# Optimization experiments

Hardware: AMD Instinct MI355X
Metric: run time of the kernel (lower is better)

Reference implementation:

```python
import jax, jax.numpy as jnp
import numpy as np

N_NODES = 50000
EPS = 1e-5


def gcn_conv(x, edge_index, edge_weight, W, b, n):
    # PyG GCNConv: h = x @ W; out[dst] += norm * h[src]; out += b
    # with self-loops (weight 1) and symmetric normalization D^-1/2 A D^-1/2.
    src, dst = edge_index[0], edge_index[1]
    loop = jnp.arange(n)
    src_all = jnp.concatenate([src, loop])            # [E+N]
    dst_all = jnp.concatenate([dst, loop])
    w_all = jnp.concatenate([edge_weight, jnp.ones((n,), x.dtype)])
    deg = jax.ops.segment_sum(w_all, dst_all, num_segments=n)
    dinv = jnp.where(deg > 0, jax.lax.rsqrt(jnp.maximum(deg, 1e-30)), 0.0)
    norm = dinv[src_all] * w_all * dinv[dst_all]      # [E+N]
    h = x @ W                                         # [N, out]
    msg = h[src_all] * norm[:, None]                  # [E+N, out]
    return jax.ops.segment_sum(msg, dst_all, num_segments=n) + b


def setup_inputs() -> dict:
    key = jax.random.key(0)
    ks = jax.random.split(key, 8)
    nfeat, nhid, nout = 1024, 256, 256
    E = 800000
    x = jax.random.normal(ks[0], (N_NODES, nfeat), dtype=jnp.float32)
    edge_index = jax.random.randint(ks[1], (2, E), 0, N_NODES, dtype=jnp.int64)
    edge_weight = jax.random.uniform(ks[2], (E,), dtype=jnp.float32)
    W1 = jax.random.normal(ks[3], (nfeat, nhid), dtype=jnp.float32) / np.sqrt(nfeat)
    b1 = jnp.zeros((nhid,), jnp.float32)
    W2 = jax.random.normal(ks[4], (nhid, nout), dtype=jnp.float32) / np.sqrt(nhid)
    b2 = jnp.zeros((nout,), jnp.float32)
    bn_gamma = jnp.ones((nout,), jnp.float32)
    bn_beta = jnp.zeros((nout,), jnp.float32)
    ln_gamma = jnp.ones((nout,), jnp.float32)
    ln_beta = jnp.zeros((nout,), jnp.float32)
    return {"x": x, "edge_index": edge_index, "edge_weight": edge_weight,
            "W1": W1, "b1": b1, "W2": W2, "b2": b2,
            "bn_gamma": bn_gamma, "bn_beta": bn_beta,
            "ln_gamma": ln_gamma, "ln_beta": ln_beta}


def reference(x, edge_index, edge_weight, W1, b1, W2, b2,
              bn_gamma, bn_beta, ln_gamma, ln_beta):
    n = x.shape[0]
    # dropout is identity in eval mode
    h = jax.nn.relu(gcn_conv(x, edge_index, edge_weight, W1, b1, n))
    h = jax.nn.relu(gcn_conv(h, edge_index, edge_weight, W2, b2, n))
    # BatchNorm1d (training-mode batch statistics, biased variance)
    mu = jnp.mean(h, axis=0)
    var = jnp.mean((h - mu) ** 2, axis=0)
    h = (h - mu) * jax.lax.rsqrt(var + EPS) * bn_gamma + bn_beta
    # LayerNorm over feature dim
    lmu = jnp.mean(h, axis=-1, keepdims=True)
    lvar = jnp.mean((h - lmu) ** 2, axis=-1, keepdims=True)
    return (h - lmu) * jax.lax.rsqrt(lvar + EPS) * ln_gamma + ln_beta
```

## Files before the change

kernel.cpp:

```cpp
#include <hip/hip_runtime.h>


typedef __attribute__((ext_vector_type(4))) float f32x4;
typedef __attribute__((ext_vector_type(8))) _Float16 f16x8;
typedef __attribute__((ext_vector_type(4))) _Float16 f16x4;

#define NN 50000
#define NF 1024
#define NH 256

__global__ __launch_bounds__(256) void deg_count(const int* __restrict__ ei,
    const float* __restrict__ ew, unsigned long long* __restrict__ dc, int E)
{
    int e = blockIdx.x * 256 + threadIdx.x;
    if (e >= E) return;
    int d = ei[E + e];
    unsigned long long pack = (1ull << 40) |
        (unsigned long long)(unsigned int)(ew[e] * 16777216.0f + 0.5f);
    atomicAdd(&dc[d], pack);
}

__global__ __launch_bounds__(256) void dinv_k(const unsigned long long* __restrict__ dc,
    float* __restrict__ dinv, int n)
{
    int i = blockIdx.x * 256 + threadIdx.x;
    if (i < n) {
        float deg = (float)(dc[i] & 0xFFFFFFFFFFull) * (1.0f / 16777216.0f);
        dinv[i] = rsqrtf(deg + 1.0f);
    }
}

__global__ __launch_bounds__(512) void scan_a(const unsigned long long* __restrict__ dc,
    int* __restrict__ excl, int* __restrict__ bsum, int n)
{
    __shared__ int sm[512];
    int t = threadIdx.x, g = blockIdx.x * 512 + t;
    int v = (g < n) ? (int)(dc[g] >> 40) : 0;
    sm[t] = v;
    __syncthreads();
    for (int d = 1; d < 512; d <<= 1) {
        int x = (t >= d) ? sm[t - d] : 0;
        __syncthreads();
        sm[t] += x;
        __syncthreads();
    }
    if (g < n) excl[g] = sm[t] - v;
    if (t == 511) bsum[blockIdx.x] = sm[511];
}

__global__ __launch_bounds__(128) void scan_b(int* __restrict__ bsum, int nb)
{
    __shared__ int sm[128];
    int t = threadIdx.x;
    int v = (t < nb) ? bsum[t] : 0;
    sm[t] = v;
    __syncthreads();
    for (int d = 1; d < 128; d <<= 1) {
        int x = (t >= d) ? sm[t - d] : 0;
        __syncthreads();
        sm[t] += x;
        __syncthreads();
    }
    if (t < nb) bsum[t] = sm[t] - v;
}

__global__ __launch_bounds__(256) void scan_c(const int* __restrict__ excl,
    const int* __restrict__ bsum, int* __restrict__ offs, int n, int E)
{
    int g = blockIdx.x * 256 + threadIdx.x;
    if (g < n) offs[g] = excl[g] + bsum[g >> 9];
    else if (g == n) offs[n] = E;
}

__global__ __launch_bounds__(256) void scatter_k(const int* __restrict__ ei,
    const float* __restrict__ ew, const int* __restrict__ offs,
    int* __restrict__ cursor, const float* __restrict__ dinv,
    int* __restrict__ csrc, float* __restrict__ cwv, int E)
{
    int e = blockIdx.x * 256 + threadIdx.x;
    if (e >= E) return;
    int s = ei[e], d = ei[E + e];
    int pos = offs[d] + atomicAdd(&cursor[d], 1);
    csrc[pos] = s;
    cwv[pos] = ew[e] * dinv[s] * dinv[d];
}

__global__ __launch_bounds__(256) void cvt_w(const float* __restrict__ W,
    unsigned short* __restrict__ WT, int K, int total)
{
    int idx = blockIdx.x * 256 + threadIdx.x;
    if (idx >= total) return;
    int k = idx >> 8, n = idx & 255;
    ((_Float16*)WT)[(size_t)n * K + k] = (_Float16)W[idx];
}

template<bool AF32>
__global__ __launch_bounds__(256, 2) void gemm_pipe(
    const void* __restrict__ Av, const unsigned short* __restrict__ BT,
    _Float16* __restrict__ C, int M, int K)
{
    constexpr int LS = 40;
    __shared__ _Float16 As[2][128 * LS];
    __shared__ _Float16 Bs[2][128 * LS];
    const int t = threadIdx.x;
    const int lane = t & 63, wid = t >> 6;
    const int r = lane & 15, q = lane >> 4;
    const int n0 = blockIdx.x * 128;
    const int m0 = blockIdx.y * 128;
    const int wm = (wid >> 1) * 64, wn = (wid & 1) * 64;
    const float* Af = (const float*)Av;
    const _Float16* Ah = (const _Float16*)Av;

    int rowA32[4], rowA16[2];
#pragma unroll
    for (int it = 0; it < 4; ++it) {
        int m = it * 32 + (t >> 3);
        int gm = m0 + m; if (gm >= M) gm = M - 1;
        rowA32[it] = gm;
    }
#pragma unroll
    for (int it = 0; it < 2; ++it) {
        int m = it * 64 + (t >> 2);
        int gm = m0 + m; if (gm >= M) gm = M - 1;
        rowA16[it] = gm;
    }
    const int kcA32 = (t & 7) << 2;
    const int kcA16 = (t & 3) << 3;
    const int nB = (t >> 2) & 63;
    const int kcB = (t & 3) << 3;

    f32x4 acc[4][4];
#pragma unroll
    for (int i = 0; i < 4; ++i)
#pragma unroll
        for (int j = 0; j < 4; ++j) acc[i][j] = (f32x4){0.f, 0.f, 0.f, 0.f};

    f32x4 apre[2][4][2];
    f16x8 aph[2][2];
    f16x8 bpre[2][2];

    const int T = K >> 5;

#define G_ISSUE_A(kt, p)                                                        \
    {                                                                           \
        if constexpr (AF32) {                                                   \
            _Pragma("unroll")                                                   \
            for (int it = 0; it < 4; ++it) {                                    \
                const float* g = Af + (size_t)rowA32[it] * K + ((kt) << 5) + kcA32; \
                apre[p][it][0] = *(const f32x4*)g;                              \
            }                                                                   \
        } else {                                                                \
            _Pragma("unroll")                                                   \
            for (int it = 0; it < 2; ++it)                                      \
                aph[p][it] = *(const f16x8*)(Ah + (size_t)rowA16[it] * K + ((kt) << 5) + kcA16); \
        }                                                                       \
    }

#define G_ISSUE_B(kt, p)                                                        \
    {                                                                           \
        _Pragma("unroll")                                                       \
        for (int rd = 0; rd < 2; ++rd)                                          \
            bpre[p][rd] = *(const f16x8*)((const _Float16*)BT +                 \
                (size_t)(n0 + rd * 64 + nB) * K + ((kt) << 5) + kcB);           \
    }

#define G_STAGE(p)                                                              \
    {                                                                           \
        if constexpr (AF32) {                                                   \
            _Pragma("unroll")                                                   \
            for (int it = 0; it < 4; ++it) {                                    \
                int m = it * 32 + (t >> 3);                                     \
                f16x4 hv;                                                       \
                hv.x = (_Float16)apre[p][it][0].x;                              \
                hv.y = (_Float16)apre[p][it][0].y;                              \
                hv.z = (_Float16)apre[p][it][0].z;                              \
                hv.w = (_Float16)apre[p][it][0].w;                              \
                *(f16x4*)(&As[p][0] + m * LS + kcA32) = hv;                     \
            }                                                                   \
        } else {                                                                \
            _Pragma("unroll")                                                   \
            for (int it = 0; it < 2; ++it) {                                    \
                int m = it * 64 + (t >> 2);                                     \
                *(f16x8*)(&As[p][0] + m * LS + kcA16) = aph[p][it];             \
            }                                                                   \
        }                                                                       \
        _Pragma("unroll")                                                       \
        for (int rd = 0; rd < 2; ++rd) {                                        \
            int n = rd * 64 + (t >> 2);                                         \
            *(f16x8*)(&Bs[p][0] + n * LS + kcB) = bpre[p][rd];                  \
        }                                                                       \
    }


#define G_BODY(kk, p)                                                           \
    {                                                                           \
        G_STAGE(p);                                                             \
        asm volatile("s_waitcnt lgkmcnt(0)" ::: "memory");                      \
        __builtin_amdgcn_s_barrier();                                           \
        __builtin_amdgcn_sched_barrier(0);                                      \
        if ((kk) + 2 < T) { G_ISSUE_A((kk) + 2, p); G_ISSUE_B((kk) + 2, p); }   \
        __builtin_amdgcn_sched_barrier(0);                                      \
        f16x8 af[4], bf[4];                                                     \
        _Pragma("unroll")                                                       \
        for (int i = 0; i < 4; ++i)                                             \
            af[i] = *(const f16x8*)(&As[p][0] + (wm + i * 16 + r) * LS + q * 8); \
        _Pragma("unroll")                                                       \
        for (int j = 0; j < 4; ++j)                                             \
            bf[j] = *(const f16x8*)(&Bs[p][0] + (wn + j * 16 + r) * LS + q * 8); \
        _Pragma("unroll")                                                       \
        for (int i = 0; i < 4; ++i)                                             \
            _Pragma("unroll")                                                   \
            for (int j = 0; j < 4; ++j)                                         \
                acc[i][j] = __builtin_amdgcn_mfma_f32_16x16x32_f16(af[i], bf[j], acc[i][j], 0, 0, 0); \
        __builtin_amdgcn_sched_barrier(0);                                      \
    }

    G_ISSUE_A(0, 0); G_ISSUE_B(0, 0);
    G_ISSUE_A(1, 1); G_ISSUE_B(1, 1);

    for (int k = 0; k < T; k += 2) {
        G_BODY(k, 0);
        G_BODY(k + 1, 1);
    }

#pragma unroll
    for (int i = 0; i < 4; ++i) {
#pragma unroll
        for (int reg = 0; reg < 4; ++reg) {
            int m = m0 + wm + i * 16 + q * 4 + reg;
            if (m < M) {
                _Float16* cp = C + (size_t)m * 256 + (n0 + wn + r);
#pragma unroll
                for (int j = 0; j < 4; ++j) cp[j * 16] = (_Float16)acc[i][j][reg];
            }
        }
    }
#undef G_ISSUE_A
#undef G_ISSUE_B
#undef G_STAGE
#undef G_BODY
}

__global__ __launch_bounds__(256) void agg_relu(
    const _Float16* __restrict__ h, const int* __restrict__ roff,
    const int* __restrict__ csrc, const float* __restrict__ cwv,
    const float* __restrict__ dinv, const float* __restrict__ bias,
    _Float16* __restrict__ out, int n)
{
    const int lane = threadIdx.x & 63, wid = threadIdx.x >> 6;
    const int i = blockIdx.x * 4 + wid;
    if (i >= n) return;
    const int c = lane << 2;
    const float di = dinv[i];
    const float sw = di * di;
    const f16x4 hv = *(const f16x4*)(h + (size_t)i * 256 + c);
    float a0 = sw * (float)hv.x, a1 = sw * (float)hv.y;
    float a2 = sw * (float)hv.z, a3 = sw * (float)hv.w;
    float b0 = 0.f, b1 = 0.f, b2 = 0.f, b3 = 0.f;
    float c0 = 0.f, c1 = 0.f, c2 = 0.f, c3 = 0.f;
    float d0 = 0.f, d1 = 0.f, d2 = 0.f, d3 = 0.f;
    const int p0 = roff[i], pe = roff[i + 1];
    for (int base = p0; base < pe; base += 64) {
        int lim = pe - base; if (lim > 64) lim = 64;
        int sv = 0; float wv = 0.f;
        if (lane < lim) { sv = csrc[base + lane]; wv = cwv[base + lane]; }
        int j = 0;
        for (; j + 3 < lim; j += 4) {
            int s0 = __shfl(sv, j),     s1 = __shfl(sv, j + 1);
            int s2 = __shfl(sv, j + 2), s3 = __shfl(sv, j + 3);
            float w0 = __shfl(wv, j),     w1 = __shfl(wv, j + 1);
            float w2 = __shfl(wv, j + 2), w3 = __shfl(wv, j + 3);
            f16x4 v0 = *(const f16x4*)(h + (size_t)s0 * 256 + c);
            f16x4 v1 = *(const f16x4*)(h + (size_t)s1 * 256 + c);
            f16x4 v2 = *(const f16x4*)(h + (size_t)s2 * 256 + c);
            f16x4 v3 = *(const f16x4*)(h + (size_t)s3 * 256 + c);
            a0 += w0 * (float)v0.x; a1 += w0 * (float)v0.y;
            a2 += w0 * (float)v0.z; a3 += w0 * (float)v0.w;
            b0 += w1 * (float)v1.x; b1 += w1 * (float)v1.y;
            b2 += w1 * (float)v1.z; b3 += w1 * (float)v1.w;
            c0 += w2 * (float)v2.x; c1 += w2 * (float)v2.y;
            c2 += w2 * (float)v2.z; c3 += w2 * (float)v2.w;
            d0 += w3 * (float)v3.x; d1 += w3 * (float)v3.y;
            d2 += w3 * (float)v3.z; d3 += w3 * (float)v3.w;
        }
        for (; j < lim; ++j) {
            int s0 = __shfl(sv, j);
            float w0 = __shfl(wv, j);
            f16x4 v0 = *(const f16x4*)(h + (size_t)s0 * 256 + c);
            a0 += w0 * (float)v0.x; a1 += w0 * (float)v0.y;
            a2 += w0 * (float)v0.z; a3 += w0 * (float)v0.w;
        }
    }
    const float4 bb = *(const float4*)(bias + c);
    f16x4 o;
    o.x = (_Float16)fmaxf(a0 + b0 + c0 + d0 + bb.x, 0.f);
    o.y = (_Float16)fmaxf(a1 + b1 + c1 + d1 + bb.y, 0.f);
    o.z = (_Float16)fmaxf(a2 + b2 + c2 + d2 + bb.z, 0.f);
    o.w = (_Float16)fmaxf(a3 + b3 + c3 + d3 + bb.w, 0.f);
    *(f16x4*)(out + (size_t)i * 256 + c) = o;
}

__global__ __launch_bounds__(256) void bn_stats(const _Float16* __restrict__ h,
    float* __restrict__ bnsum, float* __restrict__ bnsq, int n)
{
    const int t = threadIdx.x;
    float s = 0.f, s2 = 0.f;
    for (int r = blockIdx.x; r < n; r += gridDim.x) {
        float v = (float)h[(size_t)r * 256 + t];
        s += v; s2 += v * v;
    }
    atomicAdd(&bnsum[t], s);
    atomicAdd(&bnsq[t], s2);
}

__global__ __launch_bounds__(256) void bn_params(const float* __restrict__ bnsum,
    const float* __restrict__ bnsq, const float* __restrict__ gamma,
    const float* __restrict__ beta, float* __restrict__ scale,
    float* __restrict__ shift, int n)
{
    int t = threadIdx.x;
    float mu = bnsum[t] / (float)n;
    float var = bnsq[t] / (float)n - mu * mu;
    float sc = gamma[t] * rsqrtf(var + 1e-5f);
    scale[t] = sc;
    shift[t] = beta[t] - mu * sc;
}

__global__ __launch_bounds__(256) void bn_ln(const _Float16* __restrict__ h,
    const float* __restrict__ scale, const float* __restrict__ shift,
    const float* __restrict__ lng, const float* __restrict__ lnb,
    float* __restrict__ out, int n)
{
    const int lane = threadIdx.x & 63, wid = threadIdx.x >> 6;
    const int i = blockIdx.x * 4 + wid;
    if (i >= n) return;
    const int c = lane << 2;
    const f16x4 v = *(const f16x4*)(h + (size_t)i * 256 + c);
    const float4 sc = *(const float4*)(scale + c);
    const float4 sh = *(const float4*)(shift + c);
    float y0 = (float)v.x * sc.x + sh.x;
    float y1 = (float)v.y * sc.y + sh.y;
    float y2 = (float)v.z * sc.z + sh.z;
    float y3 = (float)v.w * sc.w + sh.w;
    float ps = y0 + y1 + y2 + y3;
    float ps2 = y0 * y0 + y1 * y1 + y2 * y2 + y3 * y3;
#pragma unroll
    for (int off = 32; off > 0; off >>= 1) {
        ps += __shfl_down(ps, off);
        ps2 += __shfl_down(ps2, off);
    }
    ps = __shfl(ps, 0);
    ps2 = __shfl(ps2, 0);
    const float mu = ps * (1.f / 256.f);
    const float var = ps2 * (1.f / 256.f) - mu * mu;
    const float rs = rsqrtf(var + 1e-5f);
    const float4 g = *(const float4*)(lng + c);
    const float4 bb = *(const float4*)(lnb + c);
    float4 o;
    o.x = (y0 - mu) * rs * g.x + bb.x;
    o.y = (y1 - mu) * rs * g.y + bb.y;
    o.z = (y2 - mu) * rs * g.z + bb.z;
    o.w = (y3 - mu) * rs * g.w + bb.w;
    *(float4*)(out + (size_t)i * 256 + c) = o;
}

extern "C" void kernel_launch(void* const* d_in, const int* in_sizes, int n_in,
                              void* d_out, int out_size, void* d_ws, size_t ws_size,
                              hipStream_t stream)
{
    const float* x   = (const float*)d_in[0];
    const int*   ei  = (const int*)d_in[1];
    const float* ew  = (const float*)d_in[2];
    const float* W1  = (const float*)d_in[3];
    const float* b1  = (const float*)d_in[4];
    const float* W2  = (const float*)d_in[5];
    const float* b2  = (const float*)d_in[6];
    const float* bng = (const float*)d_in[7];
    const float* bnb = (const float*)d_in[8];
    const float* lng = (const float*)d_in[9];
    const float* lnb = (const float*)d_in[10];
    float* out = (float*)d_out;

    const int N = NN;
    const int E = in_sizes[2];

    char* ws = (char*)d_ws;
    size_t o = 0;
    auto alloc = [&](size_t b) -> char* {
        char* p = ws + o;
        o = (o + b + 255) & ~(size_t)255;
        return p;
    };
    _Float16* h1  = (_Float16*)alloc((size_t)N * NH * 2);
    _Float16* h1a = (_Float16*)alloc((size_t)N * NH * 2);
    _Float16* h2a = (_Float16*)alloc((size_t)N * NH * 2);
    unsigned short* W1T = (unsigned short*)alloc((size_t)NH * NF * 2);
    unsigned short* W2T = (unsigned short*)alloc((size_t)NH * NH * 2);
    int*   csrc = (int*)alloc((size_t)E * 4);
    float* cwv  = (float*)alloc((size_t)E * 4);
    int*   offs = (int*)alloc((size_t)(N + 1) * 4);
    int*   excl = (int*)alloc((size_t)N * 4);
    int*   bsum = (int*)alloc(512);
    float* dinv = (float*)alloc((size_t)N * 4);
    float* bnscale = (float*)alloc(NH * 4);
    float* bnshift = (float*)alloc(NH * 4);
    char* zbase = ws + o;
    unsigned long long* dc = (unsigned long long*)alloc((size_t)N * 8);
    int*   cursor = (int*)alloc((size_t)N * 4);
    float* bnsum  = (float*)alloc(NH * 4);
    float* bnsq   = (float*)alloc(NH * 4);
    size_t zbytes = (size_t)((ws + o) - zbase);
    (void)hipMemsetAsync(zbase, 0, zbytes, stream);

    cvt_w<<<(NF * NH + 255) / 256, 256, 0, stream>>>(W1, W1T, NF, NF * NH);
    cvt_w<<<(NH * NH + 255) / 256, 256, 0, stream>>>(W2, W2T, NH, NH * NH);
    deg_count<<<(E + 255) / 256, 256, 0, stream>>>(ei, ew, dc, E);
    dinv_k<<<(N + 255) / 256, 256, 0, stream>>>(dc, dinv, N);
    scan_a<<<(N + 511) / 512, 512, 0, stream>>>(dc, excl, bsum, N);
    scan_b<<<1, 128, 0, stream>>>(bsum, (N + 511) / 512);
    scan_c<<<(N + 1 + 255) / 256, 256, 0, stream>>>(excl, bsum, offs, N, E);
    scatter_k<<<(E + 255) / 256, 256, 0, stream>>>(ei, ew, offs, cursor, dinv, csrc, cwv, E);

    dim3 gg(2, (N + 127) / 128);
    gemm_pipe<true><<<gg, 256, 0, stream>>>(x, W1T, h1, N, NF);
    agg_relu<<<(N + 3) / 4, 256, 0, stream>>>(h1, offs, csrc, cwv, dinv, b1, h1a, N);
    gemm_pipe<false><<<gg, 256, 0, stream>>>(h1a, W2T, h1, N, NH);
    agg_relu<<<(N + 3) / 4, 256, 0, stream>>>(h1, offs, csrc, cwv, dinv, b2, h2a, N);

    bn_stats<<<256, 256, 0, stream>>>(h2a, bnsum, bnsq, N);
    bn_params<<<1, 256, 0, stream>>>(bnsum, bnsq, bng, bnb, bnscale, bnshift, N);
    bn_ln<<<(N + 3) / 4, 256, 0, stream>>>(h2a, bnscale, bnshift, lng, lnb, out, N);
}
```

Measured before the change: 645.8 us.

## Tile weight transpose via LDS, unroll aggregation by 8, vectorize BN stats

The weight transpose-convert kernel now goes through a shared-memory tile, so both its global reads and its writes are coalesced instead of scattered strided stores. The aggregation inner loop is unrolled from 4 to 8 neighbours, with a 2-wide remainder loop, to keep more gathers in flight. bn_stats now reads four fp16 values per thread and reduces in shared memory before the atomics, giving vectorized loads and fewer atomics. The costs are more registers in agg_relu, which may lower occupancy, and extra barriers in bn_stats.

```diff
diff --git a/kernel.cpp b/kernel.cpp
--- a/kernel.cpp
+++ b/kernel.cpp
@@ -86,12 +86,31 @@
 }
 
 __global__ __launch_bounds__(256) void cvt_w(const float* __restrict__ W,
-    unsigned short* __restrict__ WT, int K, int total)
-{
-    int idx = blockIdx.x * 256 + threadIdx.x;
-    if (idx >= total) return;
-    int k = idx >> 8, n = idx & 255;
-    ((_Float16*)WT)[(size_t)n * K + k] = (_Float16)W[idx];
+    unsigned short* __restrict__ WT, int K)
+{
+    __shared__ _Float16 tile[64][72];
+    const int t = threadIdx.x;
+    const int k0 = blockIdx.x << 6, n0 = blockIdx.y << 6;
+#pragma unroll
+    for (int it = 0; it < 4; ++it) {
+        int idx = it * 256 + t;
+        int kk = idx >> 4;
+        int nn = (idx & 15) << 2;
+        float4 v = *(const float4*)(W + (size_t)(k0 + kk) * 256 + n0 + nn);
+        tile[nn + 0][kk] = (_Float16)v.x;
+        tile[nn + 1][kk] = (_Float16)v.y;
+        tile[nn + 2][kk] = (_Float16)v.z;
+        tile[nn + 3][kk] = (_Float16)v.w;
+    }
+    __syncthreads();
+#pragma unroll
+    for (int it = 0; it < 2; ++it) {
+        int idx = it * 256 + t;
+        int nn = idx >> 3;
+        int kk = (idx & 7) << 3;
+        *(f16x8*)((_Float16*)WT + (size_t)(n0 + nn) * K + k0 + kk) =
+            *(const f16x8*)&tile[nn][kk];
+    }
 }
 
 template<bool AF32>
@@ -191,7 +210,6 @@
         }                                                                       \
     }
 
-
 #define G_BODY(kk, p)                                                           \
     {                                                                           \
         G_STAGE(p);                                                             \
@@ -265,15 +283,23 @@
         int sv = 0; float wv = 0.f;
         if (lane < lim) { sv = csrc[base + lane]; wv = cwv[base + lane]; }
         int j = 0;
-        for (; j + 3 < lim; j += 4) {
+        for (; j + 7 < lim; j += 8) {
             int s0 = __shfl(sv, j),     s1 = __shfl(sv, j + 1);
             int s2 = __shfl(sv, j + 2), s3 = __shfl(sv, j + 3);
+            int s4 = __shfl(sv, j + 4), s5 = __shfl(sv, j + 5);
+            int s6 = __shfl(sv, j + 6), s7 = __shfl(sv, j + 7);
             float w0 = __shfl(wv, j),     w1 = __shfl(wv, j + 1);
             float w2 = __shfl(wv, j + 2), w3 = __shfl(wv, j + 3);
+            float w4 = __shfl(wv, j + 4), w5 = __shfl(wv, j + 5);
+            float w6 = __shfl(wv, j + 6), w7 = __shfl(wv, j + 7);
             f16x4 v0 = *(const f16x4*)(h + (size_t)s0 * 256 + c);
             f16x4 v1 = *(const f16x4*)(h + (size_t)s1 * 256 + c);
             f16x4 v2 = *(const f16x4*)(h + (size_t)s2 * 256 + c);
             f16x4 v3 = *(const f16x4*)(h + (size_t)s3 * 256 + c);
+            f16x4 v4 = *(const f16x4*)(h + (size_t)s4 * 256 + c);
+            f16x4 v5 = *(const f16x4*)(h + (size_t)s5 * 256 + c);
+            f16x4 v6 = *(const f16x4*)(h + (size_t)s6 * 256 + c);
+            f16x4 v7 = *(const f16x4*)(h + (size_t)s7 * 256 + c);
             a0 += w0 * (float)v0.x; a1 += w0 * (float)v0.y;
             a2 += w0 * (float)v0.z; a3 += w0 * (float)v0.w;
             b0 += w1 * (float)v1.x; b1 += w1 * (float)v1.y;
@@ -282,8 +308,26 @@
             c2 += w2 * (float)v2.z; c3 += w2 * (float)v2.w;
             d0 += w3 * (float)v3.x; d1 += w3 * (float)v3.y;
             d2 += w3 * (float)v3.z; d3 += w3 * (float)v3.w;
+            a0 += w4 * (float)v4.x; a1 += w4 * (float)v4.y;
+            a2 += w4 * (float)v4.z; a3 += w4 * (float)v4.w;
+            b0 += w5 * (float)v5.x; b1 += w5 * (float)v5.y;
+            b2 += w5 * (float)v5.z; b3 += w5 * (float)v5.w;
+            c0 += w6 * (float)v6.x; c1 += w6 * (float)v6.y;
+            c2 += w6 * (float)v6.z; c3 += w6 * (float)v6.w;
+            d0 += w7 * (float)v7.x; d1 += w7 * (float)v7.y;
+            d2 += w7 * (float)v7.z; d3 += w7 * (float)v7.w;
         }
-        for (; j < lim; ++j) {
+        for (; j + 1 < lim; j += 2) {
+            int s0 = __shfl(sv, j), s1 = __shfl(sv, j + 1);
+            float w0 = __shfl(wv, j), w1 = __shfl(wv, j + 1);
+            f16x4 v0 = *(const f16x4*)(h + (size_t)s0 * 256 + c);
+            f16x4 v1 = *(const f16x4*)(h + (size_t)s1 * 256 + c);
+            a0 += w0 * (float)v0.x; a1 += w0 * (float)v0.y;
+            a2 += w0 * (float)v0.z; a3 += w0 * (float)v0.w;
+            b0 += w1 * (float)v1.x; b1 += w1 * (float)v1.y;
+            b2 += w1 * (float)v1.z; b3 += w1 * (float)v1.w;
+        }
+        if (j < lim) {
             int s0 = __shfl(sv, j);
             float w0 = __shfl(wv, j);
             f16x4 v0 = *(const f16x4*)(h + (size_t)s0 * 256 + c);
@@ -303,14 +347,38 @@
 __global__ __launch_bounds__(256) void bn_stats(const _Float16* __restrict__ h,
     float* __restrict__ bnsum, float* __restrict__ bnsq, int n)
 {
-    const int t = threadIdx.x;
-    float s = 0.f, s2 = 0.f;
-    for (int r = blockIdx.x; r < n; r += gridDim.x) {
-        float v = (float)h[(size_t)r * 256 + t];
-        s += v; s2 += v * v;
-    }
-    atomicAdd(&bnsum[t], s);
-    atomicAdd(&bnsq[t], s2);
+    const int t = threadIdx.x, lane = t & 63, g = t >> 6;
+    const int c = lane << 2;
+    float s0 = 0.f, s1 = 0.f, s2 = 0.f, s3 = 0.f;
+    float q0 = 0.f, q1 = 0.f, q2 = 0.f, q3 = 0.f;
+    for (int r = blockIdx.x * 4 + g; r < n; r += gridDim.x * 4) {
+        f16x4 v = *(const f16x4*)(h + (size_t)r * 256 + c);
+        float f0 = (float)v.x, f1 = (float)v.y, f2 = (float)v.z, f3 = (float)v.w;
+        s0 += f0; s1 += f1; s2 += f2; s3 += f3;
+        q0 += f0 * f0; q1 += f1 * f1; q2 += f2 * f2; q3 += f3 * f3;
+    }
+    __shared__ float sm[4][256];
+    *(float4*)&sm[g][c] = (float4){s0, s1, s2, s3};
+    __syncthreads();
+    if (g == 0) {
+        float4 a = *(float4*)&sm[0][c], b = *(float4*)&sm[1][c];
+        float4 d = *(float4*)&sm[2][c], e = *(float4*)&sm[3][c];
+        atomicAdd(&bnsum[c + 0], a.x + b.x + d.x + e.x);
+        atomicAdd(&bnsum[c + 1], a.y + b.y + d.y + e.y);
+        atomicAdd(&bnsum[c + 2], a.z + b.z + d.z + e.z);
+        atomicAdd(&bnsum[c + 3], a.w + b.w + d.w + e.w);
+    }
+    __syncthreads();
+    *(float4*)&sm[g][c] = (float4){q0, q1, q2, q3};
+    __syncthreads();
+    if (g == 0) {
+        float4 a = *(float4*)&sm[0][c], b = *(float4*)&sm[1][c];
+        float4 d = *(float4*)&sm[2][c], e = *(float4*)&sm[3][c];
+        atomicAdd(&bnsq[c + 0], a.x + b.x + d.x + e.x);
+        atomicAdd(&bnsq[c + 1], a.y + b.y + d.y + e.y);
+        atomicAdd(&bnsq[c + 2], a.z + b.z + d.z + e.z);
+        atomicAdd(&bnsq[c + 3], a.w + b.w + d.w + e.w);
+    }
 }
 
 __global__ __launch_bounds__(256) void bn_params(const float* __restrict__ bnsum,
@@ -412,8 +480,8 @@
     size_t zbytes = (size_t)((ws + o) - zbase);
     (void)hipMemsetAsync(zbase, 0, zbytes, stream);
 
-    cvt_w<<<(NF * NH + 255) / 256, 256, 0, stream>>>(W1, W1T, NF, NF * NH);
-    cvt_w<<<(NH * NH + 255) / 256, 256, 0, stream>>>(W2, W2T, NH, NH * NH);
+    cvt_w<<<dim3(NF >> 6, 4), 256, 0, stream>>>(W1, W1T, NF);
+    cvt_w<<<dim3(NH >> 6, 4), 256, 0, stream>>>(W2, W2T, NH);
     deg_count<<<(E + 255) / 256, 256, 0, stream>>>(ei, ew, dc, E);
     dinv_k<<<(N + 255) / 256, 256, 0, stream>>>(dc, dinv, N);
     scan_a<<<(N + 511) / 512, 512, 0, stream>>>(dc, excl, bsum, N);
```

Result: no change. 633.4 us (-1.9%).
